# Kernel optimization log

Hardware: AMD Instinct MI355X
Metric: run time of the kernel (lower is better)

Reference implementation:

```python
import jax, jax.numpy as jnp
import numpy as np

N_NODES = 50000
N_EDGES = 800000
F_NODE = 92
F_EDGE = 50
HID = 128
N_LAYERS = 2


def setup_inputs() -> dict:
    key = jax.random.key(0)
    ks = jax.random.split(key, 10)
    s = 0.05
    return {
        "x": jax.random.normal(ks[0], (N_NODES, F_NODE), jnp.float32),
        "edge_attr": jax.random.uniform(ks[1], (N_EDGES, F_EDGE), jnp.float32),
        "W_in": jax.random.normal(ks[2], (F_NODE, HID), jnp.float32) * s,
        "b_in": jnp.zeros((HID,), jnp.float32),
        "Wf": jax.random.normal(ks[3], (N_LAYERS, 2 * HID + F_EDGE, HID), jnp.float32) * s,
        "bf": jnp.zeros((N_LAYERS, HID), jnp.float32),
        "Ws": jax.random.normal(ks[4], (N_LAYERS, 2 * HID + F_EDGE, HID), jnp.float32) * s,
        "bs": jnp.zeros((N_LAYERS, HID), jnp.float32),
        "Wm": jax.random.normal(ks[5], (N_LAYERS, HID, HID), jnp.float32) * s,
        "bm": jnp.zeros((N_LAYERS, HID), jnp.float32),
        "edge_index": jax.random.randint(ks[6], (2, N_EDGES), 0, N_NODES, jnp.int64),
    }


def reference(x, edge_attr, W_in, b_in, Wf, bf, Ws, bs, Wm, bm, edge_index):
    # InputLayer: Linear + ReLU (assumed)
    h = jax.nn.relu(x @ W_in + b_in)  # [N, HID]
    src = edge_index[0]  # x_j (source)
    dst = edge_index[1]  # x_i (target, aggregation index)
    for l in range(N_LAYERS):
        # CGConv: z = [x_i, x_j, e]; out = x + sum_j sigmoid(Wf z) * softplus(Ws z)
        # Split weight over the concat axis to avoid materializing z [E, 2F+D].
        Wf_i, Wf_j, Wf_e = Wf[l, :HID], Wf[l, HID:2 * HID], Wf[l, 2 * HID:]
        Ws_i, Ws_j, Ws_e = Ws[l, :HID], Ws[l, HID:2 * HID], Ws[l, 2 * HID:]
        # Precompute node-level projections, then gather per edge.
        pf = (h @ Wf_i)[dst] + (h @ Wf_j)[src] + edge_attr @ Wf_e + bf[l]
        ps = (h @ Ws_i)[dst] + (h @ Ws_j)[src] + edge_attr @ Ws_e + bs[l]
        msg = jax.nn.sigmoid(pf) * jax.nn.softplus(ps)  # [E, HID]
        agg = jax.ops.segment_sum(msg, dst, num_segments=N_NODES)
        h = h + agg  # residual ('add' aggregation, root_weight residual)
        # MultiLayerPercetronLayer: Linear + ReLU (assumed)
        h = jax.nn.relu(h @ Wm[l] + bm[l])
    return h
```

## Files before the change

kernel.cpp:

```cpp
#include <hip/hip_runtime.h>
#include <math.h>

#define NN 50000
#define NE 800000
#define FN 92
#define FE 50
#define HID 128

__device__ __forceinline__ float sigmoidf_(float x) {
    return 1.0f / (1.0f + __expf(-x));
}
__device__ __forceinline__ float softplusf_(float x) {
    return fmaxf(x, 0.0f) + __logf(1.0f + __expf(-fabsf(x)));
}
__device__ __forceinline__ float f4get(const float4& v, int i) {
    return i == 0 ? v.x : i == 1 ? v.y : i == 2 ? v.z : v.w;
}
__device__ __forceinline__ void atomAddF(float* p, float v) {
#if defined(__gfx90a__) || defined(__gfx940__) || defined(__gfx941__) || defined(__gfx942__) || defined(__gfx950__)
    unsafeAtomicAdd(p, v);
#else
    atomicAdd(p, v);
#endif
}

template<int K, int LDA, bool BIAS, bool RELU>
__global__ __launch_bounds__(256) void k_gemm(
    const float* __restrict__ A, int M,
    const float* __restrict__ B,
    const float* __restrict__ bias,
    float* __restrict__ C0, int ldc0)
{
    const int t  = threadIdx.x;
    const int r0 = blockIdx.x * 64;
    const int cb = blockIdx.y * 64;
    const int tx = t & 15;
    const int ty = t >> 4;
    const int c4 = cb + (tx << 2);
    const int rr = r0 + (ty << 2);

    int ri[4];
#pragma unroll
    for (int i = 0; i < 4; ++i) ri[i] = (rr + i < M) ? (rr + i) : 0;

    float acc[4][4] = {};
#pragma unroll 2
    for (int k = 0; k < K; k += 4) {
        float4 a[4], b[4];
#pragma unroll
        for (int i = 0; i < 4; ++i)
            a[i] = *(const float4*)&A[(size_t)ri[i] * LDA + k];
#pragma unroll
        for (int j = 0; j < 4; ++j)
            b[j] = *(const float4*)&B[(size_t)(k + j) * 128 + c4];
#pragma unroll
        for (int kk = 0; kk < 4; ++kk)
#pragma unroll
            for (int i = 0; i < 4; ++i)
#pragma unroll
                for (int j = 0; j < 4; ++j)
                    acc[i][j] = fmaf(f4get(a[i], kk), f4get(b[kk], j), acc[i][j]);
    }

    float4 bb = make_float4(0.f, 0.f, 0.f, 0.f);
    if (BIAS) bb = *(const float4*)&bias[c4];
#pragma unroll
    for (int i = 0; i < 4; ++i) {
        const int r = rr + i;
        if (r < M) {
            float4 o;
            o.x = acc[i][0] + bb.x;
            o.y = acc[i][1] + bb.y;
            o.z = acc[i][2] + bb.z;
            o.w = acc[i][3] + bb.w;
            if (RELU) {
                o.x = fmaxf(o.x, 0.f); o.y = fmaxf(o.y, 0.f);
                o.z = fmaxf(o.z, 0.f); o.w = fmaxf(o.w, 0.f);
            }
            *(float4*)&C0[(size_t)r * ldc0 + c4] = o;
        }
    }
}

__global__ __launch_bounds__(256) void k_edge_msg(
    const float* __restrict__ P,
    const float* __restrict__ ea,
    const float* __restrict__ Wfe,
    const float* __restrict__ Wse,
    const float* __restrict__ bfl,
    const float* __restrict__ bsl,
    const int*   __restrict__ esrc,
    const int*   __restrict__ edst,
    float*       __restrict__ accp)
{
    __shared__ float Wl[2 * 50 * 128];
    __shared__ float eal[32 * 50];
    __shared__ int   il[2][32];

    const int t = threadIdx.x;

    for (int idx = t; idx < 1600; idx += 256) {
        const int k = idx >> 5, cq = (idx & 31) << 2;
        *(float4*)&Wl[k * 128 + cq]        = *(const float4*)&Wfe[k * 128 + cq];
        *(float4*)&Wl[6400 + k * 128 + cq] = *(const float4*)&Wse[k * 128 + cq];
    }

    const int cq_   = t & 63;
    const int which = cq_ >> 5;
    const int c4    = (cq_ & 31) << 2;
    const int eg    = t >> 6;
    const float* bias = which ? bsl : bfl;
    const float4 bb = *(const float4*)&bias[c4];
    const float* WlW = Wl + which * 6400;
    const int pofs = which * 256;

    const int NB = NE / 32;
    for (int b = blockIdx.x; b < NB; b += gridDim.x) {
        const int e0 = b * 32;
        for (int idx = t; idx < 1600; idx += 256)
            eal[idx] = ea[(size_t)e0 * 50 + idx];
        if (t < 32)      il[0][t]      = esrc[e0 + t];
        else if (t < 64) il[1][t - 32] = edst[e0 + t - 32];
        __syncthreads();

        float m[8][4];
#pragma unroll
        for (int ii = 0; ii < 8; ++ii) {
            const int le = eg * 8 + ii;
            const int d = il[1][le], s = il[0][le];
            const float4 g1 = *(const float4*)&P[(size_t)d * 512 + pofs + c4];
            const float4 g2 = *(const float4*)&P[(size_t)s * 512 + pofs + 128 + c4];
            m[ii][0] = g1.x + g2.x + bb.x;
            m[ii][1] = g1.y + g2.y + bb.y;
            m[ii][2] = g1.z + g2.z + bb.z;
            m[ii][3] = g1.w + g2.w + bb.w;
        }
        for (int k = 0; k < 50; ++k) {
            const float4 w = *(const float4*)&WlW[k * 128 + c4];
#pragma unroll
            for (int ii = 0; ii < 8; ++ii) {
                const float e = eal[(eg * 8 + ii) * 50 + k];
                m[ii][0] = fmaf(e, w.x, m[ii][0]);
                m[ii][1] = fmaf(e, w.y, m[ii][1]);
                m[ii][2] = fmaf(e, w.z, m[ii][2]);
                m[ii][3] = fmaf(e, w.w, m[ii][3]);
            }
        }
#pragma unroll
        for (int ii = 0; ii < 8; ++ii) {
#pragma unroll
            for (int j = 0; j < 4; ++j) {
                const float v = m[ii][j];
                const float a = which ? softplusf_(v) : sigmoidf_(v);
                const float o = __shfl_xor(a, 32, 64);
                m[ii][j] = a * o;
            }
        }
        if (which == 0) {
#pragma unroll
            for (int q = 0; q < 4; ++q) {
                const int d = il[1][eg * 8 + q];
                float* p = accp + (size_t)d * 128 + c4;
                atomAddF(p + 0, m[q][0]);
                atomAddF(p + 1, m[q][1]);
                atomAddF(p + 2, m[q][2]);
                atomAddF(p + 3, m[q][3]);
            }
        } else {
#pragma unroll
            for (int q = 0; q < 4; ++q) {
                const int d = il[1][eg * 8 + 4 + q];
                float* p = accp + (size_t)d * 128 + c4;
                atomAddF(p + 0, m[4 + q][0]);
                atomAddF(p + 1, m[4 + q][1]);
                atomAddF(p + 2, m[4 + q][2]);
                atomAddF(p + 3, m[4 + q][3]);
            }
        }
        __syncthreads();
    }
}

extern "C" void kernel_launch(void* const* d_in, const int* in_sizes, int n_in,
                              void* d_out, int out_size, void* d_ws, size_t ws_size,
                              hipStream_t stream)
{
    const float* x    = (const float*)d_in[0];
    const float* ea   = (const float*)d_in[1];
    const float* W_in = (const float*)d_in[2];
    const float* b_in = (const float*)d_in[3];
    const float* Wf   = (const float*)d_in[4];
    const float* bf   = (const float*)d_in[5];
    const float* Ws   = (const float*)d_in[6];
    const float* bs   = (const float*)d_in[7];
    const float* Wm   = (const float*)d_in[8];
    const float* bm   = (const float*)d_in[9];
    const int*   ei   = (const int*)d_in[10];

    float* h   = (float*)d_ws;
    float* acc = h   + (size_t)NN * HID;
    float* P   = acc + (size_t)NN * HID;
    float* out = (float*)d_out;

    const dim3 blk(256);
    const dim3 gRows(782, 2, 1);

    k_gemm<FN, FN, true, true><<<gRows, blk, 0, stream>>>(x, NN, W_in, b_in, h, HID);

    for (int l = 0; l < 2; ++l) {
        const float* Wf_l = Wf + (size_t)l * 306 * HID;
        const float* Ws_l = Ws + (size_t)l * 306 * HID;

        k_gemm<HID, HID, false, false><<<gRows, blk, 0, stream>>>(h, NN, Wf_l,                nullptr, P + 0 * HID, 512);
        k_gemm<HID, HID, false, false><<<gRows, blk, 0, stream>>>(h, NN, Wf_l + 128 * HID,    nullptr, P + 1 * HID, 512);
        k_gemm<HID, HID, false, false><<<gRows, blk, 0, stream>>>(h, NN, Ws_l,                nullptr, P + 2 * HID, 512);
        k_gemm<HID, HID, false, false><<<gRows, blk, 0, stream>>>(h, NN, Ws_l + 128 * HID,    nullptr, P + 3 * HID, 512);

        hipMemcpyAsync(acc, h, (size_t)NN * HID * sizeof(float),
                       hipMemcpyDeviceToDevice, stream);

        k_edge_msg<<<dim3(2048), blk, 0, stream>>>(
            P, ea, Wf_l + 256 * HID, Ws_l + 256 * HID,
            bf + l * HID, bs + l * HID, ei, ei + NE, acc);

        float* c0 = (l == 1) ? out : h;
        k_gemm<HID, HID, true, true><<<gRows, blk, 0, stream>>>(
            acc, NN, Wm + (size_t)l * HID * HID, bm + l * HID, c0, HID);
    }
    (void)in_sizes; (void)n_in; (void)out_size; (void)ws_size;
}
```

Baseline: 3.848 ms.

## Merge node projection GEMMs and widen edge kernel to 64 edges per block

The four per-layer node projection GEMMs become one launch that picks the weight slice from blockIdx.y, cutting launch overhead. The edge message kernel moves to 512 threads handling 64 edges per iteration. Its edge-attribute tile is padded to a stride of 52 so the inner loop can read float4 edge features and unroll K by 4, with a two-column tail. This means fewer shared-memory loads and barriers per edge, but raises register and LDS pressure under the launch bound of 512 threads and 4 blocks per SM.

```diff
diff --git a/kernel.cpp b/kernel.cpp
--- a/kernel.cpp
+++ b/kernel.cpp
@@ -25,15 +25,14 @@
 }
 
 template<int K, int LDA, bool BIAS, bool RELU>
-__global__ __launch_bounds__(256) void k_gemm(
+__device__ __forceinline__ void gemm_body(
     const float* __restrict__ A, int M,
     const float* __restrict__ B,
     const float* __restrict__ bias,
-    float* __restrict__ C0, int ldc0)
+    float* __restrict__ C0, int ldc0,
+    int r0, int cb)
 {
     const int t  = threadIdx.x;
-    const int r0 = blockIdx.x * 64;
-    const int cb = blockIdx.y * 64;
     const int tx = t & 15;
     const int ty = t >> 4;
     const int c4 = cb + (tx << 2);
@@ -82,7 +81,31 @@
     }
 }
 
-__global__ __launch_bounds__(256) void k_edge_msg(
+template<int K, int LDA, bool BIAS, bool RELU>
+__global__ __launch_bounds__(256) void k_gemm(
+    const float* __restrict__ A, int M,
+    const float* __restrict__ B,
+    const float* __restrict__ bias,
+    float* __restrict__ C0, int ldc0)
+{
+    gemm_body<K, LDA, BIAS, RELU>(A, M, B, bias, C0, ldc0,
+                                  blockIdx.x * 64, blockIdx.y * 64);
+}
+
+__global__ __launch_bounds__(256) void k_gemm_p(
+    const float* __restrict__ h,
+    const float* __restrict__ Bf,
+    const float* __restrict__ Bs,
+    float* __restrict__ P)
+{
+    const int mm = blockIdx.y >> 1;
+    const float* B = (mm < 2) ? (Bf + (size_t)mm * 128 * HID)
+                              : (Bs + (size_t)(mm - 2) * 128 * HID);
+    gemm_body<HID, HID, false, false>(h, NN, B, nullptr, P + mm * HID, 512,
+                                      blockIdx.x * 64, (blockIdx.y & 1) * 64);
+}
+
+__global__ __launch_bounds__(512, 4) void k_edge_msg(
     const float* __restrict__ P,
     const float* __restrict__ ea,
     const float* __restrict__ Wfe,
@@ -94,40 +117,40 @@
     float*       __restrict__ accp)
 {
     __shared__ float Wl[2 * 50 * 128];
-    __shared__ float eal[32 * 50];
-    __shared__ int   il[2][32];
+    __shared__ float eal[64 * 52];
+    __shared__ int   il0[64], il1[64];
 
     const int t = threadIdx.x;
 
-    for (int idx = t; idx < 1600; idx += 256) {
+    for (int idx = t; idx < 1600; idx += 512) {
         const int k = idx >> 5, cq = (idx & 31) << 2;
         *(float4*)&Wl[k * 128 + cq]        = *(const float4*)&Wfe[k * 128 + cq];
         *(float4*)&Wl[6400 + k * 128 + cq] = *(const float4*)&Wse[k * 128 + cq];
     }
 
-    const int cq_   = t & 63;
-    const int which = cq_ >> 5;
-    const int c4    = (cq_ & 31) << 2;
-    const int eg    = t >> 6;
-    const float* bias = which ? bsl : bfl;
-    const float4 bb = *(const float4*)&bias[c4];
-    const float* WlW = Wl + which * 6400;
-    const int pofs = which * 256;
-
-    const int NB = NE / 32;
+    const int half = (t & 63) >> 5;
+    const int c4   = (t & 31) << 2;
+    const int eg   = t >> 6;
+    const float4 bb = *(const float4*)&((half ? bsl : bfl)[c4]);
+    const float* WlW = Wl + half * 6400;
+    const int pofs = half * 256;
+
+    const int NB = NE / 64;
     for (int b = blockIdx.x; b < NB; b += gridDim.x) {
-        const int e0 = b * 32;
-        for (int idx = t; idx < 1600; idx += 256)
-            eal[idx] = ea[(size_t)e0 * 50 + idx];
-        if (t < 32)      il[0][t]      = esrc[e0 + t];
-        else if (t < 64) il[1][t - 32] = edst[e0 + t - 32];
+        const int e0 = b * 64;
+        for (int idx = t; idx < 64 * 50; idx += 512) {
+            const int r = idx / 50;
+            eal[r * 52 + (idx - r * 50)] = ea[(size_t)e0 * 50 + idx];
+        }
+        if (t < 64)       il0[t]      = esrc[e0 + t];
+        else if (t < 128) il1[t - 64] = edst[e0 + t - 64];
         __syncthreads();
 
         float m[8][4];
 #pragma unroll
         for (int ii = 0; ii < 8; ++ii) {
             const int le = eg * 8 + ii;
-            const int d = il[1][le], s = il[0][le];
+            const int d = il1[le], s = il0[le];
             const float4 g1 = *(const float4*)&P[(size_t)d * 512 + pofs + c4];
             const float4 g2 = *(const float4*)&P[(size_t)s * 512 + pofs + 128 + c4];
             m[ii][0] = g1.x + g2.x + bb.x;
@@ -135,15 +158,46 @@
             m[ii][2] = g1.z + g2.z + bb.z;
             m[ii][3] = g1.w + g2.w + bb.w;
         }
-        for (int k = 0; k < 50; ++k) {
-            const float4 w = *(const float4*)&WlW[k * 128 + c4];
+        for (int k = 0; k < 48; k += 4) {
+            const float4 w0 = *(const float4*)&WlW[(k + 0) * 128 + c4];
+            const float4 w1 = *(const float4*)&WlW[(k + 1) * 128 + c4];
+            const float4 w2 = *(const float4*)&WlW[(k + 2) * 128 + c4];
+            const float4 w3 = *(const float4*)&WlW[(k + 3) * 128 + c4];
 #pragma unroll
             for (int ii = 0; ii < 8; ++ii) {
-                const float e = eal[(eg * 8 + ii) * 50 + k];
-                m[ii][0] = fmaf(e, w.x, m[ii][0]);
-                m[ii][1] = fmaf(e, w.y, m[ii][1]);
-                m[ii][2] = fmaf(e, w.z, m[ii][2]);
-                m[ii][3] = fmaf(e, w.w, m[ii][3]);
+                const float4 ev = *(const float4*)&eal[(eg * 8 + ii) * 52 + k];
+                m[ii][0] = fmaf(ev.x, w0.x, m[ii][0]);
+                m[ii][1] = fmaf(ev.x, w0.y, m[ii][1]);
+                m[ii][2] = fmaf(ev.x, w0.z, m[ii][2]);
+                m[ii][3] = fmaf(ev.x, w0.w, m[ii][3]);
+                m[ii][0] = fmaf(ev.y, w1.x, m[ii][0]);
+                m[ii][1] = fmaf(ev.y, w1.y, m[ii][1]);
+                m[ii][2] = fmaf(ev.y, w1.z, m[ii][2]);
+                m[ii][3] = fmaf(ev.y, w1.w, m[ii][3]);
+                m[ii][0] = fmaf(ev.z, w2.x, m[ii][0]);
+                m[ii][1] = fmaf(ev.z, w2.y, m[ii][1]);
+                m[ii][2] = fmaf(ev.z, w2.z, m[ii][2]);
+                m[ii][3] = fmaf(ev.z, w2.w, m[ii][3]);
+                m[ii][0] = fmaf(ev.w, w3.x, m[ii][0]);
+                m[ii][1] = fmaf(ev.w, w3.y, m[ii][1]);
+                m[ii][2] = fmaf(ev.w, w3.z, m[ii][2]);
+                m[ii][3] = fmaf(ev.w, w3.w, m[ii][3]);
+            }
+        }
+        {
+            const float4 w0 = *(const float4*)&WlW[48 * 128 + c4];
+            const float4 w1 = *(const float4*)&WlW[49 * 128 + c4];
+#pragma unroll
+            for (int ii = 0; ii < 8; ++ii) {
+                const float2 ev = *(const float2*)&eal[(eg * 8 + ii) * 52 + 48];
+                m[ii][0] = fmaf(ev.x, w0.x, m[ii][0]);
+                m[ii][1] = fmaf(ev.x, w0.y, m[ii][1]);
+                m[ii][2] = fmaf(ev.x, w0.z, m[ii][2]);
+                m[ii][3] = fmaf(ev.x, w0.w, m[ii][3]);
+                m[ii][0] = fmaf(ev.y, w1.x, m[ii][0]);
+                m[ii][1] = fmaf(ev.y, w1.y, m[ii][1]);
+                m[ii][2] = fmaf(ev.y, w1.z, m[ii][2]);
+                m[ii][3] = fmaf(ev.y, w1.w, m[ii][3]);
             }
         }
 #pragma unroll
@@ -151,15 +205,15 @@
 #pragma unroll
             for (int j = 0; j < 4; ++j) {
                 const float v = m[ii][j];
-                const float a = which ? softplusf_(v) : sigmoidf_(v);
+                const float a = half ? softplusf_(v) : sigmoidf_(v);
                 const float o = __shfl_xor(a, 32, 64);
                 m[ii][j] = a * o;
             }
         }
-        if (which == 0) {
+        if (half == 0) {
 #pragma unroll
             for (int q = 0; q < 4; ++q) {
-                const int d = il[1][eg * 8 + q];
+                const int d = il1[eg * 8 + q];
                 float* p = accp + (size_t)d * 128 + c4;
                 atomAddF(p + 0, m[q][0]);
                 atomAddF(p + 1, m[q][1]);
@@ -169,7 +223,7 @@
         } else {
 #pragma unroll
             for (int q = 0; q < 4; ++q) {
-                const int d = il[1][eg * 8 + 4 + q];
+                const int d = il1[eg * 8 + 4 + q];
                 float* p = accp + (size_t)d * 128 + c4;
                 atomAddF(p + 0, m[4 + q][0]);
                 atomAddF(p + 1, m[4 + q][1]);
@@ -211,15 +265,12 @@
         const float* Wf_l = Wf + (size_t)l * 306 * HID;
         const float* Ws_l = Ws + (size_t)l * 306 * HID;
 
-        k_gemm<HID, HID, false, false><<<gRows, blk, 0, stream>>>(h, NN, Wf_l,                nullptr, P + 0 * HID, 512);
-        k_gemm<HID, HID, false, false><<<gRows, blk, 0, stream>>>(h, NN, Wf_l + 128 * HID,    nullptr, P + 1 * HID, 512);
-        k_gemm<HID, HID, false, false><<<gRows, blk, 0, stream>>>(h, NN, Ws_l,                nullptr, P + 2 * HID, 512);
-        k_gemm<HID, HID, false, false><<<gRows, blk, 0, stream>>>(h, NN, Ws_l + 128 * HID,    nullptr, P + 3 * HID, 512);
+        k_gemm_p<<<dim3(782, 8), blk, 0, stream>>>(h, Wf_l, Ws_l, P);
 
         hipMemcpyAsync(acc, h, (size_t)NN * HID * sizeof(float),
                        hipMemcpyDeviceToDevice, stream);
 
-        k_edge_msg<<<dim3(2048), blk, 0, stream>>>(
+        k_edge_msg<<<dim3(2048), dim3(512), 0, stream>>>(
             P, ea, Wf_l + 256 * HID, Ws_l + 256 * HID,
             bf + l * HID, bs + l * HID, ei, ei + NE, acc);
 
```

New measurement: 3.623 ms. -5.8%, faster.
